# Performance work log

Measured on AMD Instinct MI355X. Metric: run time of the kernel, lower is better.

## Reference

```python
import jax, jax.numpy as jnp
import numpy as np

B, L, D, H = 2, 2048, 1024, 16
DH = D // H
EPS = 1e-5


def setup_inputs() -> dict:
    key = jax.random.key(0)
    ks = jax.random.split(key, 8)
    s = 0.02  # realistic init scale for weights
    # causal mask: True where attention is DISALLOWED (masked_fill semantics)
    mask = jnp.triu(jnp.ones((L, L), dtype=bool), k=1)[None, None]  # [1,1,L,L]
    return {
        "x": jax.random.normal(ks[0], (B, L, D), jnp.float32),
        "mask": mask,
        "ln_g": jnp.ones((D,), jnp.float32),
        "ln_b": jnp.zeros((D,), jnp.float32),
        "Wq": jax.random.normal(ks[1], (D, D), jnp.float32) * s,
        "bq": jnp.zeros((D,), jnp.float32),
        "Wk": jax.random.normal(ks[2], (D, D), jnp.float32) * s,
        "bk": jnp.zeros((D,), jnp.float32),
        "Wv": jax.random.normal(ks[3], (D, D), jnp.float32) * s,
        "bv": jnp.zeros((D,), jnp.float32),
        "Wo": jax.random.normal(ks[4], (D, D), jnp.float32) * s,
        "bo": jnp.zeros((D,), jnp.float32),
    }


def _layernorm(x, g, b):
    mu = jnp.mean(x, axis=-1, keepdims=True)
    var = jnp.var(x, axis=-1, keepdims=True)
    return (x - mu) * jax.lax.rsqrt(var + EPS) * g + b


def reference(x, mask, ln_g, ln_b, Wq, bq, Wk, bk, Wv, bv, Wo, bo):
    b, l, d = x.shape
    h = _layernorm(x, ln_g, ln_b)
    # separate Q/K/V linears, split into heads: [b, H, l, DH]
    q = (h @ Wq + bq).reshape(b, l, H, DH).transpose(0, 2, 1, 3)
    k = (h @ Wk + bk).reshape(b, l, H, DH).transpose(0, 2, 1, 3)
    v = (h @ Wv + bv).reshape(b, l, H, DH).transpose(0, 2, 1, 3)
    scale = jnp.asarray(DH, x.dtype) ** -0.5
    # full L x L score matrix (this is exactly what the torch module does)
    w = jnp.einsum("bhqd,bhkd->bhqk", q, k) * scale
    w = jnp.where(mask, -jnp.inf, w)
    w = jax.nn.softmax(w, axis=-1)
    # dropout layers are identity in eval mode
    o = jnp.einsum("bhqk,bhkd->bhqd", w, v)
    o = o.transpose(0, 2, 1, 3).reshape(b, l, d)
    return o @ Wo + bo
```

## Files before the change

kernel.cpp:

```cpp
#include <hip/hip_runtime.h>
#include <hip/hip_bf16.h>


typedef __bf16  bf16x8 __attribute__((ext_vector_type(8)));
typedef __bf16  bf16x4 __attribute__((ext_vector_type(4)));
typedef float   f32x4  __attribute__((ext_vector_type(4)));
typedef float   f32x16 __attribute__((ext_vector_type(16)));

#define MFMA16(a, b, c) __builtin_amdgcn_mfma_f32_16x16x32_bf16(a, b, c, 0, 0, 0)
#define MFMA32(a, b, c) __builtin_amdgcn_mfma_f32_32x32x16_bf16(a, b, c, 0, 0, 0)

#define LDT 72
#define LDP 72
#define LDO 68

#define QSCALE 0.18033688011112042f

__device__ __forceinline__ void gl_lds16(const void* g, void* l) {
    __builtin_amdgcn_global_load_lds(
        (const __attribute__((address_space(1))) void*)g,
        (__attribute__((address_space(3))) void*)l, 16, 0, 0);
}

__global__ __launch_bounds__(256) void ln_kernel(
    const float* __restrict__ x, const float* __restrict__ g,
    const float* __restrict__ bta, __hip_bfloat16* __restrict__ h)
{
    __shared__ float red[8];
    const int row = blockIdx.x, t = threadIdx.x;
    const float* xr = x + (size_t)row * 1024;
    const float4 xv = *(const float4*)(xr + t * 4);
    float s  = xv.x + xv.y + xv.z + xv.w;
    float ss = xv.x * xv.x + xv.y * xv.y + xv.z * xv.z + xv.w * xv.w;
    #pragma unroll
    for (int off = 32; off > 0; off >>= 1) {
        s  += __shfl_down(s, off);
        ss += __shfl_down(ss, off);
    }
    const int lane = t & 63, wave = t >> 6;
    if (lane == 0) { red[wave] = s; red[4 + wave] = ss; }
    __syncthreads();
    const float S  = red[0] + red[1] + red[2] + red[3];
    const float SS = red[4] + red[5] + red[6] + red[7];
    const float mu   = S * (1.0f / 1024.0f);
    const float var  = SS * (1.0f / 1024.0f) - mu * mu;
    const float rstd = rsqrtf(var + 1e-5f);
    const float4 gv = *(const float4*)(g + t * 4);
    const float4 bv = *(const float4*)(bta + t * 4);
    bf16x4 hv;
    hv[0] = (__bf16)((xv.x - mu) * rstd * gv.x + bv.x);
    hv[1] = (__bf16)((xv.y - mu) * rstd * gv.y + bv.y);
    hv[2] = (__bf16)((xv.z - mu) * rstd * gv.z + bv.z);
    hv[3] = (__bf16)((xv.w - mu) * rstd * gv.w + bv.w);
    *(bf16x4*)(h + (size_t)row * 1024 + t * 4) = hv;
}

__global__ void transpose_cast_kernel(
    const float* __restrict__ Wq, const float* __restrict__ Wk,
    const float* __restrict__ Wv, const float* __restrict__ Wo,
    __hip_bfloat16* __restrict__ tq, __hip_bfloat16* __restrict__ tk,
    __hip_bfloat16* __restrict__ tv, __hip_bfloat16* __restrict__ to_)
{
    __shared__ float t[32][33];
    const int z = blockIdx.z;
    const float* src = (z == 0) ? Wq : (z == 1) ? Wk : (z == 2) ? Wv : Wo;
    __hip_bfloat16* dst = (z == 0) ? tq : (z == 1) ? tk : (z == 2) ? tv : to_;
    const int n0 = blockIdx.x * 32, k0 = blockIdx.y * 32;
    const int tx = threadIdx.x, ty = threadIdx.y;
    t[ty][tx] = src[(size_t)(k0 + ty) * 1024 + n0 + tx];
    __syncthreads();
    dst[(size_t)(n0 + ty) * 1024 + k0 + tx] = __float2bfloat16(t[tx][ty]);
}

__device__ __forceinline__ void gemm_core_1024(
    const __hip_bfloat16* __restrict__ A, const __hip_bfloat16* __restrict__ Bt,
    int m0, int n0, f32x4 (&acc)[4][2])
{
    __shared__ __align__(16) __hip_bfloat16 sA[128 * 32];
    __shared__ __align__(16) __hip_bfloat16 sB[128 * 32];
    const int tid  = threadIdx.x;
    const int wave = tid >> 6, lane = tid & 63;
    const int quad = lane >> 4, l16 = lane & 15;
    const int wm = wave >> 2, wn = wave & 3;

    const f32x4 zero = {0.f, 0.f, 0.f, 0.f};
    #pragma unroll
    for (int i = 0; i < 4; ++i)
        #pragma unroll
        for (int j = 0; j < 2; ++j) acc[i][j] = zero;

    const int r0 = tid >> 2, cc = (tid & 3) << 3;
    const __hip_bfloat16* Ap = A  + (size_t)(m0 + r0) * 1024 + cc;
    const __hip_bfloat16* Bp = Bt + (size_t)(n0 + r0) * 1024 + cc;
    __hip_bfloat16* lA0 = sA + r0 * 32 + cc;
    __hip_bfloat16* lB0 = sB + r0 * 32 + cc;

    for (int k0 = 0; k0 < 1024; k0 += 32) {
        __syncthreads();
        gl_lds16(Ap + k0, lA0);
        gl_lds16(Bp + k0, lB0);
        __syncthreads();
        bf16x8 af[4], bfr[2];
        #pragma unroll
        for (int mt = 0; mt < 4; ++mt)
            af[mt] = *(const bf16x8*)(sA + (wm * 64 + mt * 16 + l16) * 32 + quad * 8);
        #pragma unroll
        for (int nt = 0; nt < 2; ++nt)
            bfr[nt] = *(const bf16x8*)(sB + (wn * 32 + nt * 16 + l16) * 32 + quad * 8);
        #pragma unroll
        for (int mt = 0; mt < 4; ++mt)
            #pragma unroll
            for (int nt = 0; nt < 2; ++nt)
                acc[mt][nt] = MFMA16(af[mt], bfr[nt], acc[mt][nt]);
    }
}

__global__ __launch_bounds__(512) void gemm_qkv_kernel(
    const __hip_bfloat16* __restrict__ h,
    const __hip_bfloat16* __restrict__ wt_base,
    const float* __restrict__ bq, const float* __restrict__ bk,
    const float* __restrict__ bv,
    __hip_bfloat16* __restrict__ qkv_base)
{
    const int z = blockIdx.z;
    const __hip_bfloat16* wt = wt_base + ((size_t)z << 20);
    __hip_bfloat16* outp = qkv_base + ((size_t)z << 22);

    const bool swp = (z == 2);
    const __hip_bfloat16* A  = swp ? wt : h;
    const __hip_bfloat16* Bt = swp ? h  : wt;
    const int m0 = swp ? blockIdx.x * 128 : blockIdx.y * 128;
    const int n0 = swp ? blockIdx.y * 128 : blockIdx.x * 128;

    f32x4 acc[4][2];
    gemm_core_1024(A, Bt, m0, n0, acc);

    const int lane = threadIdx.x & 63, wave = threadIdx.x >> 6;
    const int quad = lane >> 4, l16 = lane & 15;
    const int wm = wave >> 2, wn = wave & 3;

    if (!swp) {
        const float* bias = (z == 0) ? bq : bk;
        const float scale = (z == 0) ? QSCALE : 1.0f;
        #pragma unroll
        for (int mt = 0; mt < 4; ++mt)
            #pragma unroll
            for (int nt = 0; nt < 2; ++nt)
                #pragma unroll
                for (int r = 0; r < 4; ++r) {
                    const int gm = m0 + wm * 64 + mt * 16 + quad * 4 + r;
                    const int gn = n0 + wn * 32 + nt * 16 + l16;
                    const float v = (acc[mt][nt][r] + bias[gn]) * scale;
                    const int b = gm >> 11, l = gm & 2047;
                    const int hh = gn >> 6, dh = gn & 63;
                    outp[(((((size_t)(b * 16 + hh)) << 11) + l) * 64) + dh] = __float2bfloat16(v);
                }
    } else {
        #pragma unroll
        for (int mt = 0; mt < 4; ++mt)
            #pragma unroll
            for (int nt = 0; nt < 2; ++nt)
                #pragma unroll
                for (int r = 0; r < 4; ++r) {
                    const int rr = m0 + wm * 64 + mt * 16 + quad * 4 + r;
                    const int cc = n0 + wn * 32 + nt * 16 + l16;
                    const float v = acc[mt][nt][r] + bv[rr];
                    const int b = cc >> 11, l = cc & 2047;
                    const int hh = rr >> 6, dh = rr & 63;
                    outp[((((size_t)(b * 16 + hh)) * 64 + dh) << 11) + l] = __float2bfloat16(v);
                }
    }
}

__global__ __launch_bounds__(512) void gemm_out_kernel(
    const __hip_bfloat16* __restrict__ o, const __hip_bfloat16* __restrict__ wot,
    const float* __restrict__ bo, float* __restrict__ out)
{
    __shared__ __align__(16) __hip_bfloat16 sA[64 * 32];
    __shared__ __align__(16) __hip_bfloat16 sB[128 * 32];
    const int tid  = threadIdx.x;
    const int wave = tid >> 6, lane = tid & 63;
    const int quad = lane >> 4, l16 = lane & 15;
    const int wm = wave >> 2, wn = wave & 3;
    const int m0 = blockIdx.y * 64, n0 = blockIdx.x * 128;

    const f32x4 zero = {0.f, 0.f, 0.f, 0.f};
    f32x4 acc[2][2];
    #pragma unroll
    for (int i = 0; i < 2; ++i)
        #pragma unroll
        for (int j = 0; j < 2; ++j) acc[i][j] = zero;

    const int r0 = tid >> 2, cc = (tid & 3) << 3;
    const __hip_bfloat16* Ap = o   + (size_t)(m0 + r0) * 1024 + cc;
    const __hip_bfloat16* Bp = wot + (size_t)(n0 + r0) * 1024 + cc;
    __hip_bfloat16* lA0 = sA + r0 * 32 + cc;
    __hip_bfloat16* lB0 = sB + r0 * 32 + cc;

    for (int k0 = 0; k0 < 1024; k0 += 32) {
        __syncthreads();
        if (tid < 256) gl_lds16(Ap + k0, lA0);
        gl_lds16(Bp + k0, lB0);
        __syncthreads();
        bf16x8 af[2], bfr[2];
        #pragma unroll
        for (int mt = 0; mt < 2; ++mt)
            af[mt] = *(const bf16x8*)(sA + (wm * 32 + mt * 16 + l16) * 32 + quad * 8);
        #pragma unroll
        for (int nt = 0; nt < 2; ++nt)
            bfr[nt] = *(const bf16x8*)(sB + (wn * 32 + nt * 16 + l16) * 32 + quad * 8);
        #pragma unroll
        for (int mt = 0; mt < 2; ++mt)
            #pragma unroll
            for (int nt = 0; nt < 2; ++nt)
                acc[mt][nt] = MFMA16(af[mt], bfr[nt], acc[mt][nt]);
    }

    #pragma unroll
    for (int mt = 0; mt < 2; ++mt)
        #pragma unroll
        for (int nt = 0; nt < 2; ++nt)
            #pragma unroll
            for (int r = 0; r < 4; ++r) {
                const int gm = m0 + wm * 32 + mt * 16 + quad * 4 + r;
                const int gn = n0 + wn * 32 + nt * 16 + l16;
                out[(size_t)gm * 1024 + gn] = acc[mt][nt][r] + bo[gn];
            }
}

__global__ __launch_bounds__(512, 4) void attn_kernel(
    const __hip_bfloat16* __restrict__ Q,
    const __hip_bfloat16* __restrict__ Kg,
    const __hip_bfloat16* __restrict__ Vt,
    __hip_bfloat16* __restrict__ O)
{
    __shared__ __align__(16) char smem[55296];
    __hip_bfloat16* sK = (__hip_bfloat16*)smem;
    __hip_bfloat16* sV = (__hip_bfloat16*)(smem + 18432);
    __hip_bfloat16* sP = (__hip_bfloat16*)(smem + 36864);

    const int tid  = threadIdx.x;
    const int wave = tid >> 6, lane = tid & 63;
    const int grp  = wave >> 2, w4 = wave & 3;
    const int wk = w4 >> 1, wq = w4 & 1;
    const int q5 = lane & 31, hi = lane >> 5;
    const int bh = blockIdx.x, pi = blockIdx.y;
    const int qtA = 31 - pi, qtB = pi;
    const int q0A = qtA * 64, q0B = qtB * 64;

    const __hip_bfloat16* Qp = Q  + (size_t)bh * 2048 * 64;
    const __hip_bfloat16* Kp = Kg + (size_t)bh * 2048 * 64;
    const __hip_bfloat16* Vp = Vt + (size_t)bh * 64 * 2048;

    bf16x8 QfA[4], QfB[4];
    #pragma unroll
    for (int ks = 0; ks < 4; ++ks) {
        QfA[ks] = *(const bf16x8*)(Qp + (size_t)(q0A + wq * 32 + q5) * 64 + ks * 16 + hi * 8);
        QfB[ks] = *(const bf16x8*)(Qp + (size_t)(q0B + wq * 32 + q5) * 64 + ks * 16 + hi * 8);
    }

    f32x16 oA, oB;
    #pragma unroll
    for (int r = 0; r < 16; ++r) { oA[r] = 0.f; oB[r] = 0.f; }
    float lA = 0.f, lB = 0.f;

    const __hip_bfloat16* sKg = sK + grp * (64 * LDT);
    const __hip_bfloat16* sVg = sV + grp * (64 * LDT);
    __hip_bfloat16*       sPg = sP + grp * (64 * LDP);
    const int qloc = wq * 32 + q5;

    const int sg = tid >> 8, tt = tid & 255;

    auto phase1 = [&](const bf16x8 (&Qf)[4], float& l_run, bool diag) {
        f32x16 s;
        #pragma unroll
        for (int i = 0; i < 16; ++i) s[i] = 0.f;
        #pragma unroll
        for (int ks = 0; ks < 4; ++ks) {
            const bf16x8 kf = *(const bf16x8*)(sKg + (wk * 32 + q5) * LDT + ks * 16 + hi * 8);
            s = MFMA32(kf, Qf[ks], s);
        }
        if (diag) {
            #pragma unroll
            for (int i = 0; i < 16; ++i) {
                const int krow = wk * 32 + (i & 3) + 8 * (i >> 2) + 4 * hi;
                if (krow > qloc) s[i] = -1e30f;
            }
        }
        float rs = 0.f;
        #pragma unroll
        for (int rb = 0; rb < 4; ++rb) {
            bf16x4 pk;
            #pragma unroll
            for (int i = 0; i < 4; ++i) {
                const float p = exp2f(s[rb * 4 + i]);
                rs += p;
                pk[i] = (__bf16)p;
            }
            *(bf16x4*)(sPg + (wq * 32 + q5) * LDP + wk * 32 + 8 * rb + 4 * hi) = pk;
        }
        rs += __shfl_xor(rs, 32);
        l_run += rs;
    };
    auto phase2 = [&](f32x16& oacc) {
        #pragma unroll
        for (int ks = 0; ks < 4; ++ks) {
            const bf16x8 vf = *(const bf16x8*)(sVg + (wk * 32 + q5) * LDT + ks * 16 + hi * 8);
            const bf16x8 pf = *(const bf16x8*)(sPg + (wq * 32 + q5) * LDP + ks * 16 + hi * 8);
            oacc = MFMA32(vf, pf, oacc);
        }
    };

    for (int r = 0; r < 17; ++r) {
        __syncthreads();
        const int js = 2 * r + sg;
        if (js < 33) {
            const int ktS = (js <= qtA) ? js : js - qtA - 1;
            const int k0 = ktS * 64;
            __hip_bfloat16* dK = sK + sg * (64 * LDT);
            __hip_bfloat16* dV = sV + sg * (64 * LDT);
            #pragma unroll
            for (int i = 0; i < 2; ++i) {
                const int chunk = tt + 256 * i, rr = chunk >> 3, cc = (chunk & 7) << 3;
                *(int4*)(dK + rr * LDT + cc) = *(const int4*)(Kp + (size_t)(k0 + rr) * 64 + cc);
                *(int4*)(dV + rr * LDT + cc) = *(const int4*)(Vp + (size_t)rr * 2048 + k0 + cc);
            }
        }
        __syncthreads();

        const int j = 2 * r + grp;
        const bool act = (j < 33);
        const bool isA = act && (j <= qtA);
        if (act) {
            const int kt = isA ? j : j - qtA - 1;
            const bool diag = isA ? (kt == qtA) : (kt == qtB);
            if (isA) phase1(QfA, lA, diag);
            else     phase1(QfB, lB, diag);
        }
        __syncthreads();

        if (act) {
            if (isA) phase2(oA);
            else     phase2(oB);
        }
    }

    __syncthreads();
    float* Oscr = (float*)smem;
    float* lscr = (float*)(smem + 34816);

    if (grp == 1) {
        #pragma unroll
        for (int t2 = 0; t2 < 2; ++t2) {
            const f32x16& oc = t2 ? oB : oA;
            float* rowp = Oscr + (t2 * 64 + wq * 32 + q5) * LDO;
            #pragma unroll
            for (int rb = 0; rb < 4; ++rb) {
                f32x4 v = {oc[rb * 4 + 0], oc[rb * 4 + 1], oc[rb * 4 + 2], oc[rb * 4 + 3]};
                *(f32x4*)(rowp + wk * 32 + 8 * rb + 4 * hi) = v;
            }
        }
    }
    if (hi == 0) {
        lscr[((0 * 2 + grp) * 2 + wk) * 64 + wq * 32 + q5] = lA;
        lscr[((1 * 2 + grp) * 2 + wk) * 64 + wq * 32 + q5] = lB;
    }
    __syncthreads();
    if (grp == 0) {
        #pragma unroll
        for (int t2 = 0; t2 < 2; ++t2) {
            const f32x16& oc = t2 ? oB : oA;
            float* rowp = Oscr + (t2 * 64 + wq * 32 + q5) * LDO;
            #pragma unroll
            for (int rb = 0; rb < 4; ++rb) {
                float* p = rowp + wk * 32 + 8 * rb + 4 * hi;
                f32x4 v = *(const f32x4*)p;
                v[0] += oc[rb * 4 + 0]; v[1] += oc[rb * 4 + 1];
                v[2] += oc[rb * 4 + 2]; v[3] += oc[rb * 4 + 3];
                *(f32x4*)p = v;
            }
        }
    }
    __syncthreads();

    const int b = bh >> 4, hh = bh & 15;
    #pragma unroll
    for (int i = 0; i < 2; ++i) {
        const int chunk = tid + 512 * i;
        const int row = chunk >> 3, t2 = row >> 6, q = row & 63;
        const int col = (chunk & 7) << 3;
        const float lt = lscr[((t2 * 2 + 0) * 2 + 0) * 64 + q]
                       + lscr[((t2 * 2 + 0) * 2 + 1) * 64 + q]
                       + lscr[((t2 * 2 + 1) * 2 + 0) * 64 + q]
                       + lscr[((t2 * 2 + 1) * 2 + 1) * 64 + q];
        const float linv = 1.0f / lt;
        const float* src = Oscr + (t2 * 64 + q) * LDO + col;
        const f32x4 v0 = *(const f32x4*)src;
        const f32x4 v1 = *(const f32x4*)(src + 4);
        bf16x8 ov;
        ov[0] = (__bf16)(v0[0] * linv); ov[1] = (__bf16)(v0[1] * linv);
        ov[2] = (__bf16)(v0[2] * linv); ov[3] = (__bf16)(v0[3] * linv);
        ov[4] = (__bf16)(v1[0] * linv); ov[5] = (__bf16)(v1[1] * linv);
        ov[6] = (__bf16)(v1[2] * linv); ov[7] = (__bf16)(v1[3] * linv);
        const int q0X = t2 ? q0B : q0A;
        *(bf16x8*)(O + ((size_t)b * 2048 + q0X + q) * 1024 + hh * 64 + col) = ov;
    }
}

extern "C" void kernel_launch(void* const* d_in, const int* in_sizes, int n_in,
                              void* d_out, int out_size, void* d_ws, size_t ws_size,
                              hipStream_t stream) {
    const float* x    = (const float*)d_in[0];
    const float* ln_g = (const float*)d_in[2];
    const float* ln_b = (const float*)d_in[3];
    const float* Wq = (const float*)d_in[4];  const float* bq = (const float*)d_in[5];
    const float* Wk = (const float*)d_in[6];  const float* bk = (const float*)d_in[7];
    const float* Wv = (const float*)d_in[8];  const float* bv = (const float*)d_in[9];
    const float* Wo = (const float*)d_in[10]; const float* bo = (const float*)d_in[11];
    float* out = (float*)d_out;

    __hip_bfloat16* ws = (__hip_bfloat16*)d_ws;
    const size_t M1 = 1024 * 1024;
    __hip_bfloat16* h   = ws;
    __hip_bfloat16* wqt = ws + 4 * M1;
    __hip_bfloat16* wot = ws + 7 * M1;
    __hip_bfloat16* q   = ws + 8 * M1;
    __hip_bfloat16* k   = ws + 12 * M1;
    __hip_bfloat16* vt  = ws + 16 * M1;
    __hip_bfloat16* o   = h;

    ln_kernel<<<4096, 256, 0, stream>>>(x, ln_g, ln_b, h);
    transpose_cast_kernel<<<dim3(32, 32, 4), dim3(32, 32), 0, stream>>>(
        Wq, Wk, Wv, Wo, wqt, wqt + M1, wqt + 2 * M1, wot);
    gemm_qkv_kernel<<<dim3(8, 32, 3), 512, 0, stream>>>(h, wqt, bq, bk, bv, q);
    attn_kernel<<<dim3(32, 16), 512, 0, stream>>>(q, k, vt, o);
    gemm_out_kernel<<<dim3(8, 64), 512, 0, stream>>>(o, wot, bo, out);
}
```

Before: 205.4 us.

## Keep attention P in registers, deepen GEMM K-tile to 64 with XOR swizzle

The GEMM kernels now load 64-wide K tiles, one barrier pair per tile, into an XOR-swizzled LDS layout. This halves the number of barriers and is meant to avoid bank conflicts on the fragment reads. The attention kernel drops the shared P buffer and the barrier between the score and PV phases. It rebuilds the P operand with cross-lane shuffles, has each wave accumulate over its own key half into two output accumulators, and raises wave priority around the MFMAs. The cost is twice the accumulator registers, which puts occupancy at 4 blocks of 512 at risk, plus a four-step serialized reduction of the outputs at the end.

```diff
diff --git a/kernel.cpp b/kernel.cpp
--- a/kernel.cpp
+++ b/kernel.cpp
@@ -6,12 +6,13 @@
 typedef __bf16  bf16x4 __attribute__((ext_vector_type(4)));
 typedef float   f32x4  __attribute__((ext_vector_type(4)));
 typedef float   f32x16 __attribute__((ext_vector_type(16)));
+typedef unsigned int u32x2 __attribute__((ext_vector_type(2)));
+typedef unsigned int u32x4 __attribute__((ext_vector_type(4)));
 
 #define MFMA16(a, b, c) __builtin_amdgcn_mfma_f32_16x16x32_bf16(a, b, c, 0, 0, 0)
 #define MFMA32(a, b, c) __builtin_amdgcn_mfma_f32_32x32x16_bf16(a, b, c, 0, 0, 0)
 
 #define LDT 72
-#define LDP 72
 #define LDO 68
 
 #define QSCALE 0.18033688011112042f
@@ -76,8 +77,8 @@
     const __hip_bfloat16* __restrict__ A, const __hip_bfloat16* __restrict__ Bt,
     int m0, int n0, f32x4 (&acc)[4][2])
 {
-    __shared__ __align__(16) __hip_bfloat16 sA[128 * 32];
-    __shared__ __align__(16) __hip_bfloat16 sB[128 * 32];
+    __shared__ __align__(16) __hip_bfloat16 sA[128 * 64];
+    __shared__ __align__(16) __hip_bfloat16 sB[128 * 64];
     const int tid  = threadIdx.x;
     const int wave = tid >> 6, lane = tid & 63;
     const int quad = lane >> 4, l16 = lane & 15;
@@ -89,29 +90,38 @@
         #pragma unroll
         for (int j = 0; j < 2; ++j) acc[i][j] = zero;
 
-    const int r0 = tid >> 2, cc = (tid & 3) << 3;
-    const __hip_bfloat16* Ap = A  + (size_t)(m0 + r0) * 1024 + cc;
-    const __hip_bfloat16* Bp = Bt + (size_t)(n0 + r0) * 1024 + cc;
-    __hip_bfloat16* lA0 = sA + r0 * 32 + cc;
-    __hip_bfloat16* lB0 = sB + r0 * 32 + cc;
-
-    for (int k0 = 0; k0 < 1024; k0 += 32) {
+    const int r0 = tid >> 3;
+    const int c0 = (((tid & 7) ^ (r0 & 7)) << 3);
+    const __hip_bfloat16* Ap = A  + (size_t)(m0 + r0) * 1024 + c0;
+    const __hip_bfloat16* Bp = Bt + (size_t)(n0 + r0) * 1024 + c0;
+    __hip_bfloat16* lA0 = sA + tid * 8;
+    __hip_bfloat16* lB0 = sB + tid * 8;
+
+    const int rsw = l16 & 7;
+
+    for (int k0 = 0; k0 < 1024; k0 += 64) {
         __syncthreads();
         gl_lds16(Ap + k0, lA0);
+        gl_lds16(Ap + (size_t)64 * 1024 + k0, lA0 + 64 * 64);
         gl_lds16(Bp + k0, lB0);
-        __syncthreads();
-        bf16x8 af[4], bfr[2];
-        #pragma unroll
-        for (int mt = 0; mt < 4; ++mt)
-            af[mt] = *(const bf16x8*)(sA + (wm * 64 + mt * 16 + l16) * 32 + quad * 8);
-        #pragma unroll
-        for (int nt = 0; nt < 2; ++nt)
-            bfr[nt] = *(const bf16x8*)(sB + (wn * 32 + nt * 16 + l16) * 32 + quad * 8);
-        #pragma unroll
-        for (int mt = 0; mt < 4; ++mt)
+        gl_lds16(Bp + (size_t)64 * 1024 + k0, lB0 + 64 * 64);
+        __syncthreads();
+        #pragma unroll
+        for (int kk = 0; kk < 64; kk += 32) {
+            const int sl = (((quad + (kk >> 3)) ^ rsw) << 3);
+            bf16x8 af[4], bfr[2];
+            #pragma unroll
+            for (int mt = 0; mt < 4; ++mt)
+                af[mt] = *(const bf16x8*)(sA + (wm * 64 + mt * 16 + l16) * 64 + sl);
             #pragma unroll
             for (int nt = 0; nt < 2; ++nt)
-                acc[mt][nt] = MFMA16(af[mt], bfr[nt], acc[mt][nt]);
+                bfr[nt] = *(const bf16x8*)(sB + (wn * 32 + nt * 16 + l16) * 64 + sl);
+            #pragma unroll
+            for (int mt = 0; mt < 4; ++mt)
+                #pragma unroll
+                for (int nt = 0; nt < 2; ++nt)
+                    acc[mt][nt] = MFMA16(af[mt], bfr[nt], acc[mt][nt]);
+        }
     }
 }
 
@@ -176,8 +186,8 @@
     const __hip_bfloat16* __restrict__ o, const __hip_bfloat16* __restrict__ wot,
     const float* __restrict__ bo, float* __restrict__ out)
 {
-    __shared__ __align__(16) __hip_bfloat16 sA[64 * 32];
-    __shared__ __align__(16) __hip_bfloat16 sB[128 * 32];
+    __shared__ __align__(16) __hip_bfloat16 sA[64 * 64];
+    __shared__ __align__(16) __hip_bfloat16 sB[128 * 64];
     const int tid  = threadIdx.x;
     const int wave = tid >> 6, lane = tid & 63;
     const int quad = lane >> 4, l16 = lane & 15;
@@ -191,29 +201,37 @@
         #pragma unroll
         for (int j = 0; j < 2; ++j) acc[i][j] = zero;
 
-    const int r0 = tid >> 2, cc = (tid & 3) << 3;
-    const __hip_bfloat16* Ap = o   + (size_t)(m0 + r0) * 1024 + cc;
-    const __hip_bfloat16* Bp = wot + (size_t)(n0 + r0) * 1024 + cc;
-    __hip_bfloat16* lA0 = sA + r0 * 32 + cc;
-    __hip_bfloat16* lB0 = sB + r0 * 32 + cc;
-
-    for (int k0 = 0; k0 < 1024; k0 += 32) {
-        __syncthreads();
-        if (tid < 256) gl_lds16(Ap + k0, lA0);
+    const int r0 = tid >> 3;
+    const int c0 = (((tid & 7) ^ (r0 & 7)) << 3);
+    const __hip_bfloat16* Ap = o   + (size_t)(m0 + r0) * 1024 + c0;
+    const __hip_bfloat16* Bp = wot + (size_t)(n0 + r0) * 1024 + c0;
+    __hip_bfloat16* lA0 = sA + tid * 8;
+    __hip_bfloat16* lB0 = sB + tid * 8;
+
+    const int rsw = l16 & 7;
+
+    for (int k0 = 0; k0 < 1024; k0 += 64) {
+        __syncthreads();
+        gl_lds16(Ap + k0, lA0);
         gl_lds16(Bp + k0, lB0);
-        __syncthreads();
-        bf16x8 af[2], bfr[2];
-        #pragma unroll
-        for (int mt = 0; mt < 2; ++mt)
-            af[mt] = *(const bf16x8*)(sA + (wm * 32 + mt * 16 + l16) * 32 + quad * 8);
-        #pragma unroll
-        for (int nt = 0; nt < 2; ++nt)
-            bfr[nt] = *(const bf16x8*)(sB + (wn * 32 + nt * 16 + l16) * 32 + quad * 8);
-        #pragma unroll
-        for (int mt = 0; mt < 2; ++mt)
+        gl_lds16(Bp + (size_t)64 * 1024 + k0, lB0 + 64 * 64);
+        __syncthreads();
+        #pragma unroll
+        for (int kk = 0; kk < 64; kk += 32) {
+            const int sl = (((quad + (kk >> 3)) ^ rsw) << 3);
+            bf16x8 af[2], bfr[2];
+            #pragma unroll
+            for (int mt = 0; mt < 2; ++mt)
+                af[mt] = *(const bf16x8*)(sA + (wm * 32 + mt * 16 + l16) * 64 + sl);
             #pragma unroll
             for (int nt = 0; nt < 2; ++nt)
-                acc[mt][nt] = MFMA16(af[mt], bfr[nt], acc[mt][nt]);
+                bfr[nt] = *(const bf16x8*)(sB + (wn * 32 + nt * 16 + l16) * 64 + sl);
+            #pragma unroll
+            for (int mt = 0; mt < 2; ++mt)
+                #pragma unroll
+                for (int nt = 0; nt < 2; ++nt)
+                    acc[mt][nt] = MFMA16(af[mt], bfr[nt], acc[mt][nt]);
+        }
     }
 
     #pragma unroll
@@ -234,10 +252,9 @@
     const __hip_bfloat16* __restrict__ Vt,
     __hip_bfloat16* __restrict__ O)
 {
-    __shared__ __align__(16) char smem[55296];
+    __shared__ __align__(16) char smem[36864];
     __hip_bfloat16* sK = (__hip_bfloat16*)smem;
     __hip_bfloat16* sV = (__hip_bfloat16*)(smem + 18432);
-    __hip_bfloat16* sP = (__hip_bfloat16*)(smem + 36864);
 
     const int tid  = threadIdx.x;
     const int wave = tid >> 6, lane = tid & 63;
@@ -259,27 +276,29 @@
         QfB[ks] = *(const bf16x8*)(Qp + (size_t)(q0B + wq * 32 + q5) * 64 + ks * 16 + hi * 8);
     }
 
-    f32x16 oA, oB;
-    #pragma unroll
-    for (int r = 0; r < 16; ++r) { oA[r] = 0.f; oB[r] = 0.f; }
+    f32x16 oA0, oA1, oB0, oB1;
+    #pragma unroll
+    for (int r = 0; r < 16; ++r) { oA0[r] = 0.f; oA1[r] = 0.f; oB0[r] = 0.f; oB1[r] = 0.f; }
     float lA = 0.f, lB = 0.f;
 
     const __hip_bfloat16* sKg = sK + grp * (64 * LDT);
     const __hip_bfloat16* sVg = sV + grp * (64 * LDT);
-    __hip_bfloat16*       sPg = sP + grp * (64 * LDP);
     const int qloc = wq * 32 + q5;
 
     const int sg = tid >> 8, tt = tid & 255;
 
-    auto phase1 = [&](const bf16x8 (&Qf)[4], float& l_run, bool diag) {
+    auto do_job = [&](const bf16x8 (&Qf)[4], float& l_run, bool diag,
+                      f32x16& o0, f32x16& o1) {
         f32x16 s;
         #pragma unroll
         for (int i = 0; i < 16; ++i) s[i] = 0.f;
+        __builtin_amdgcn_s_setprio(1);
         #pragma unroll
         for (int ks = 0; ks < 4; ++ks) {
             const bf16x8 kf = *(const bf16x8*)(sKg + (wk * 32 + q5) * LDT + ks * 16 + hi * 8);
             s = MFMA32(kf, Qf[ks], s);
         }
+        __builtin_amdgcn_s_setprio(0);
         if (diag) {
             #pragma unroll
             for (int i = 0; i < 16; ++i) {
@@ -288,27 +307,39 @@
             }
         }
         float rs = 0.f;
+        u32x2 U[4];
         #pragma unroll
         for (int rb = 0; rb < 4; ++rb) {
             bf16x4 pk;
             #pragma unroll
-            for (int i = 0; i < 4; ++i) {
-                const float p = exp2f(s[rb * 4 + i]);
+            for (int c = 0; c < 4; ++c) {
+                const float p = exp2f(s[rb * 4 + c]);
                 rs += p;
-                pk[i] = (__bf16)p;
+                pk[c] = (__bf16)p;
             }
-            *(bf16x4*)(sPg + (wq * 32 + q5) * LDP + wk * 32 + 8 * rb + 4 * hi) = pk;
+            U[rb] = __builtin_bit_cast(u32x2, pk);
         }
         rs += __shfl_xor(rs, 32);
         l_run += rs;
-    };
-    auto phase2 = [&](f32x16& oacc) {
-        #pragma unroll
-        for (int ks = 0; ks < 4; ++ks) {
-            const bf16x8 vf = *(const bf16x8*)(sVg + (wk * 32 + q5) * LDT + ks * 16 + hi * 8);
-            const bf16x8 pf = *(const bf16x8*)(sPg + (wq * 32 + q5) * LDP + ks * 16 + hi * 8);
-            oacc = MFMA32(vf, pf, oacc);
-        }
+        __builtin_amdgcn_s_setprio(1);
+        #pragma unroll
+        for (int t = 0; t < 2; ++t) {
+            const unsigned p0a = __shfl_xor(U[2 * t][0], 32);
+            const unsigned p0b = __shfl_xor(U[2 * t][1], 32);
+            const unsigned p1a = __shfl_xor(U[2 * t + 1][0], 32);
+            const unsigned p1b = __shfl_xor(U[2 * t + 1][1], 32);
+            const unsigned w0 = hi ? p1a : U[2 * t][0];
+            const unsigned w1 = hi ? p1b : U[2 * t][1];
+            const unsigned w2 = hi ? U[2 * t + 1][0] : p0a;
+            const unsigned w3 = hi ? U[2 * t + 1][1] : p0b;
+            const u32x4 pw = {w0, w1, w2, w3};
+            const bf16x8 pf = __builtin_bit_cast(bf16x8, pw);
+            const bf16x8 vf0 = *(const bf16x8*)(sVg + (q5)      * LDT + wk * 32 + 16 * t + 8 * hi);
+            const bf16x8 vf1 = *(const bf16x8*)(sVg + (32 + q5) * LDT + wk * 32 + 16 * t + 8 * hi);
+            o0 = MFMA32(vf0, pf, o0);
+            o1 = MFMA32(vf1, pf, o1);
+        }
+        __builtin_amdgcn_s_setprio(0);
     };
 
     for (int r = 0; r < 17; ++r) {
@@ -329,19 +360,12 @@
         __syncthreads();
 
         const int j = 2 * r + grp;
-        const bool act = (j < 33);
-        const bool isA = act && (j <= qtA);
-        if (act) {
+        if (j < 33) {
+            const bool isA = (j <= qtA);
             const int kt = isA ? j : j - qtA - 1;
             const bool diag = isA ? (kt == qtA) : (kt == qtB);
-            if (isA) phase1(QfA, lA, diag);
-            else     phase1(QfB, lB, diag);
-        }
-        __syncthreads();
-
-        if (act) {
-            if (isA) phase2(oA);
-            else     phase2(oB);
+            if (isA) do_job(QfA, lA, diag, oA0, oA1);
+            else     do_job(QfB, lB, diag, oB0, oB1);
         }
     }
 
@@ -349,38 +373,39 @@
     float* Oscr = (float*)smem;
     float* lscr = (float*)(smem + 34816);
 
-    if (grp == 1) {
-        #pragma unroll
-        for (int t2 = 0; t2 < 2; ++t2) {
-            const f32x16& oc = t2 ? oB : oA;
-            float* rowp = Oscr + (t2 * 64 + wq * 32 + q5) * LDO;
-            #pragma unroll
-            for (int rb = 0; rb < 4; ++rb) {
-                f32x4 v = {oc[rb * 4 + 0], oc[rb * 4 + 1], oc[rb * 4 + 2], oc[rb * 4 + 3]};
-                *(f32x4*)(rowp + wk * 32 + 8 * rb + 4 * hi) = v;
-            }
-        }
-    }
     if (hi == 0) {
         lscr[((0 * 2 + grp) * 2 + wk) * 64 + wq * 32 + q5] = lA;
         lscr[((1 * 2 + grp) * 2 + wk) * 64 + wq * 32 + q5] = lB;
     }
-    __syncthreads();
-    if (grp == 0) {
-        #pragma unroll
-        for (int t2 = 0; t2 < 2; ++t2) {
-            const f32x16& oc = t2 ? oB : oA;
-            float* rowp = Oscr + (t2 * 64 + wq * 32 + q5) * LDO;
+
+    auto wrO = [&](const f32x16& c0, const f32x16& c1, int t2, bool add) {
+        float* rowp = Oscr + (t2 * 64 + wq * 32 + q5) * LDO;
+        #pragma unroll
+        for (int d = 0; d < 2; ++d) {
+            const f32x16& oc = d ? c1 : c0;
             #pragma unroll
             for (int rb = 0; rb < 4; ++rb) {
-                float* p = rowp + wk * 32 + 8 * rb + 4 * hi;
-                f32x4 v = *(const f32x4*)p;
-                v[0] += oc[rb * 4 + 0]; v[1] += oc[rb * 4 + 1];
-                v[2] += oc[rb * 4 + 2]; v[3] += oc[rb * 4 + 3];
+                float* p = rowp + d * 32 + 8 * rb + 4 * hi;
+                f32x4 v;
+                if (add) {
+                    v = *(const f32x4*)p;
+                    v[0] += oc[rb * 4 + 0]; v[1] += oc[rb * 4 + 1];
+                    v[2] += oc[rb * 4 + 2]; v[3] += oc[rb * 4 + 3];
+                } else {
+                    v[0] = oc[rb * 4 + 0]; v[1] = oc[rb * 4 + 1];
+                    v[2] = oc[rb * 4 + 2]; v[3] = oc[rb * 4 + 3];
+                }
                 *(f32x4*)p = v;
             }
         }
-    }
+    };
+    if (grp == 1 && wk == 1) { wrO(oA0, oA1, 0, false); wrO(oB0, oB1, 1, false); }
+    __syncthreads();
+    if (grp == 1 && wk == 0) { wrO(oA0, oA1, 0, true);  wrO(oB0, oB1, 1, true); }
+    __syncthreads();
+    if (grp == 0 && wk == 1) { wrO(oA0, oA1, 0, true);  wrO(oB0, oB1, 1, true); }
+    __syncthreads();
+    if (grp == 0 && wk == 0) { wrO(oA0, oA1, 0, true);  wrO(oB0, oB1, 1, true); }
     __syncthreads();
 
     const int b = bh >> 4, hh = bh & 15;
```

Result: slower. 222.8 us (+8.5%).

## Deepen GEMM K-tile to 64 with XOR-swizzled LDS and prioritize attention MFMA

Applied to the files above, without the earlier changes.

Both GEMM kernels now stage a 64-wide K slice per iteration instead of 32, halving the number of barrier pairs per output tile. Each thread loads more rows, and the LDS rows are XOR-swizzled by row so the 128-byte rows do not cause bank conflicts when fragments are read. The attention kernel also wraps its MFMA sections in s_setprio to raise wave priority during matrix work. The cost is double the shared memory per GEMM block, which may reduce occupancy.

```diff
diff --git a/kernel.cpp b/kernel.cpp
--- a/kernel.cpp
+++ b/kernel.cpp
@@ -76,8 +76,8 @@
     const __hip_bfloat16* __restrict__ A, const __hip_bfloat16* __restrict__ Bt,
     int m0, int n0, f32x4 (&acc)[4][2])
 {
-    __shared__ __align__(16) __hip_bfloat16 sA[128 * 32];
-    __shared__ __align__(16) __hip_bfloat16 sB[128 * 32];
+    __shared__ __align__(16) __hip_bfloat16 sA[128 * 64];
+    __shared__ __align__(16) __hip_bfloat16 sB[128 * 64];
     const int tid  = threadIdx.x;
     const int wave = tid >> 6, lane = tid & 63;
     const int quad = lane >> 4, l16 = lane & 15;
@@ -89,29 +89,38 @@
         #pragma unroll
         for (int j = 0; j < 2; ++j) acc[i][j] = zero;
 
-    const int r0 = tid >> 2, cc = (tid & 3) << 3;
-    const __hip_bfloat16* Ap = A  + (size_t)(m0 + r0) * 1024 + cc;
-    const __hip_bfloat16* Bp = Bt + (size_t)(n0 + r0) * 1024 + cc;
-    __hip_bfloat16* lA0 = sA + r0 * 32 + cc;
-    __hip_bfloat16* lB0 = sB + r0 * 32 + cc;
-
-    for (int k0 = 0; k0 < 1024; k0 += 32) {
+    const int r0 = tid >> 3;
+    const int c0 = (((tid & 7) ^ (r0 & 7)) << 3);
+    const __hip_bfloat16* Ap = A  + (size_t)(m0 + r0) * 1024 + c0;
+    const __hip_bfloat16* Bp = Bt + (size_t)(n0 + r0) * 1024 + c0;
+    __hip_bfloat16* lA0 = sA + tid * 8;
+    __hip_bfloat16* lB0 = sB + tid * 8;
+
+    const int rsw = l16 & 7;
+
+    for (int k0 = 0; k0 < 1024; k0 += 64) {
         __syncthreads();
         gl_lds16(Ap + k0, lA0);
+        gl_lds16(Ap + (size_t)64 * 1024 + k0, lA0 + 64 * 64);
         gl_lds16(Bp + k0, lB0);
-        __syncthreads();
-        bf16x8 af[4], bfr[2];
-        #pragma unroll
-        for (int mt = 0; mt < 4; ++mt)
-            af[mt] = *(const bf16x8*)(sA + (wm * 64 + mt * 16 + l16) * 32 + quad * 8);
-        #pragma unroll
-        for (int nt = 0; nt < 2; ++nt)
-            bfr[nt] = *(const bf16x8*)(sB + (wn * 32 + nt * 16 + l16) * 32 + quad * 8);
-        #pragma unroll
-        for (int mt = 0; mt < 4; ++mt)
+        gl_lds16(Bp + (size_t)64 * 1024 + k0, lB0 + 64 * 64);
+        __syncthreads();
+        #pragma unroll
+        for (int kk = 0; kk < 64; kk += 32) {
+            const int sl = (((quad + (kk >> 3)) ^ rsw) << 3);
+            bf16x8 af[4], bfr[2];
+            #pragma unroll
+            for (int mt = 0; mt < 4; ++mt)
+                af[mt] = *(const bf16x8*)(sA + (wm * 64 + mt * 16 + l16) * 64 + sl);
             #pragma unroll
             for (int nt = 0; nt < 2; ++nt)
-                acc[mt][nt] = MFMA16(af[mt], bfr[nt], acc[mt][nt]);
+                bfr[nt] = *(const bf16x8*)(sB + (wn * 32 + nt * 16 + l16) * 64 + sl);
+            #pragma unroll
+            for (int mt = 0; mt < 4; ++mt)
+                #pragma unroll
+                for (int nt = 0; nt < 2; ++nt)
+                    acc[mt][nt] = MFMA16(af[mt], bfr[nt], acc[mt][nt]);
+        }
     }
 }
 
@@ -176,8 +185,8 @@
     const __hip_bfloat16* __restrict__ o, const __hip_bfloat16* __restrict__ wot,
     const float* __restrict__ bo, float* __restrict__ out)
 {
-    __shared__ __align__(16) __hip_bfloat16 sA[64 * 32];
-    __shared__ __align__(16) __hip_bfloat16 sB[128 * 32];
+    __shared__ __align__(16) __hip_bfloat16 sA[64 * 64];
+    __shared__ __align__(16) __hip_bfloat16 sB[128 * 64];
     const int tid  = threadIdx.x;
     const int wave = tid >> 6, lane = tid & 63;
     const int quad = lane >> 4, l16 = lane & 15;
@@ -191,29 +200,37 @@
         #pragma unroll
         for (int j = 0; j < 2; ++j) acc[i][j] = zero;
 
-    const int r0 = tid >> 2, cc = (tid & 3) << 3;
-    const __hip_bfloat16* Ap = o   + (size_t)(m0 + r0) * 1024 + cc;
-    const __hip_bfloat16* Bp = wot + (size_t)(n0 + r0) * 1024 + cc;
-    __hip_bfloat16* lA0 = sA + r0 * 32 + cc;
-    __hip_bfloat16* lB0 = sB + r0 * 32 + cc;
-
-    for (int k0 = 0; k0 < 1024; k0 += 32) {
-        __syncthreads();
-        if (tid < 256) gl_lds16(Ap + k0, lA0);
+    const int r0 = tid >> 3;
+    const int c0 = (((tid & 7) ^ (r0 & 7)) << 3);
+    const __hip_bfloat16* Ap = o   + (size_t)(m0 + r0) * 1024 + c0;
+    const __hip_bfloat16* Bp = wot + (size_t)(n0 + r0) * 1024 + c0;
+    __hip_bfloat16* lA0 = sA + tid * 8;
+    __hip_bfloat16* lB0 = sB + tid * 8;
+
+    const int rsw = l16 & 7;
+
+    for (int k0 = 0; k0 < 1024; k0 += 64) {
+        __syncthreads();
+        gl_lds16(Ap + k0, lA0);
         gl_lds16(Bp + k0, lB0);
-        __syncthreads();
-        bf16x8 af[2], bfr[2];
-        #pragma unroll
-        for (int mt = 0; mt < 2; ++mt)
-            af[mt] = *(const bf16x8*)(sA + (wm * 32 + mt * 16 + l16) * 32 + quad * 8);
-        #pragma unroll
-        for (int nt = 0; nt < 2; ++nt)
-            bfr[nt] = *(const bf16x8*)(sB + (wn * 32 + nt * 16 + l16) * 32 + quad * 8);
-        #pragma unroll
-        for (int mt = 0; mt < 2; ++mt)
+        gl_lds16(Bp + (size_t)64 * 1024 + k0, lB0 + 64 * 64);
+        __syncthreads();
+        #pragma unroll
+        for (int kk = 0; kk < 64; kk += 32) {
+            const int sl = (((quad + (kk >> 3)) ^ rsw) << 3);
+            bf16x8 af[2], bfr[2];
+            #pragma unroll
+            for (int mt = 0; mt < 2; ++mt)
+                af[mt] = *(const bf16x8*)(sA + (wm * 32 + mt * 16 + l16) * 64 + sl);
             #pragma unroll
             for (int nt = 0; nt < 2; ++nt)
-                acc[mt][nt] = MFMA16(af[mt], bfr[nt], acc[mt][nt]);
+                bfr[nt] = *(const bf16x8*)(sB + (wn * 32 + nt * 16 + l16) * 64 + sl);
+            #pragma unroll
+            for (int mt = 0; mt < 2; ++mt)
+                #pragma unroll
+                for (int nt = 0; nt < 2; ++nt)
+                    acc[mt][nt] = MFMA16(af[mt], bfr[nt], acc[mt][nt]);
+        }
     }
 
     #pragma unroll
@@ -275,11 +292,13 @@
         f32x16 s;
         #pragma unroll
         for (int i = 0; i < 16; ++i) s[i] = 0.f;
+        __builtin_amdgcn_s_setprio(1);
         #pragma unroll
         for (int ks = 0; ks < 4; ++ks) {
             const bf16x8 kf = *(const bf16x8*)(sKg + (wk * 32 + q5) * LDT + ks * 16 + hi * 8);
             s = MFMA32(kf, Qf[ks], s);
         }
+        __builtin_amdgcn_s_setprio(0);
         if (diag) {
             #pragma unroll
             for (int i = 0; i < 16; ++i) {
@@ -303,12 +322,14 @@
         l_run += rs;
     };
     auto phase2 = [&](f32x16& oacc) {
+        __builtin_amdgcn_s_setprio(1);
         #pragma unroll
         for (int ks = 0; ks < 4; ++ks) {
             const bf16x8 vf = *(const bf16x8*)(sVg + (wk * 32 + q5) * LDT + ks * 16 + hi * 8);
             const bf16x8 pf = *(const bf16x8*)(sPg + (wq * 32 + q5) * LDP + ks * 16 + hi * 8);
             oacc = MFMA32(vf, pf, oacc);
         }
+        __builtin_amdgcn_s_setprio(0);
     };
 
     for (int r = 0; r < 17; ++r) {
```

After: 191.4 us. -6.8%, faster.
